# Optimization experiments

Measured on AMD Instinct MI355X. Metric: run time of the kernel, lower is better.

Reference implementation:

```python
import jax, jax.numpy as jnp
import numpy as np
from jax import lax

B, S, H = 2, 512, 2048          # batch, seq, hidden_size
I = 768                          # moe_intermediate_size
E = 64                           # num_experts
K = 8                            # num_experts_per_tok (top_k)


def setup_inputs() -> dict:
    key = jax.random.key(0)
    k1, k2, k3, k4 = jax.random.split(key, 4)
    hidden_states = jax.random.normal(k1, (B, S, H), jnp.float32)
    gate_weight = jax.random.normal(k2, (E, H), jnp.float32) * 0.02
    gate_up_weights = jax.random.normal(k3, (E, H, 2 * I), jnp.float32) * 0.02
    down_weights = jax.random.normal(k4, (E, I, H), jnp.float32) * 0.02
    return {
        "hidden_states": hidden_states,
        "gate_weight": gate_weight,
        "gate_up_weights": gate_up_weights,
        "down_weights": down_weights,
    }


def reference(hidden_states, gate_weight, gate_up_weights, down_weights):
    orig_shape = hidden_states.shape
    x = hidden_states.reshape(-1, H)          # [T, H]
    T = x.shape[0]

    # Router: softmax in fp32, top-k, renormalize (norm_topk_prob=True)
    logits = x @ gate_weight.T                # [T, E]
    probs = jax.nn.softmax(logits.astype(jnp.float32), axis=-1)
    routing_weights, selected_experts = lax.top_k(probs, K)   # [T, K]
    wsum = routing_weights.sum(axis=-1, keepdims=True)
    wsum = jnp.where(wsum == 0, 1.0, wsum)
    routing_weights = (routing_weights / wsum).astype(x.dtype)

    # Dense combine matrix [T, E]: zero weight for unselected experts.
    combine = jnp.zeros((T, E), x.dtype).at[
        jnp.arange(T)[:, None], selected_experts
    ].add(routing_weights)

    # Scan over experts; each step is one batched GEMM over all tokens,
    # masked/weighted by the combine weights (same math as per-token loop).
    def body(acc, ws):
        wgu, wd, we = ws                      # [H,2I], [I,H], [T]
        gu = x @ wgu                          # [T, 2I]
        gate, up = jnp.split(gu, 2, axis=-1)  # [T, I] each
        act = jax.nn.silu(gate) * up          # SwiGLU
        out = act @ wd                        # [T, H]
        return acc + we[:, None] * out, None

    init = jnp.zeros_like(x)
    final, _ = lax.scan(body, init, (gate_up_weights, down_weights, combine.T))
    return final.reshape(orig_shape)
```

## Files before the change

kernel.cpp:

```cpp
#include <hip/hip_runtime.h>
#include <hip/hip_bf16.h>
#include <hip/hip_fp16.h>

typedef unsigned int uint32;
typedef unsigned short u16;

#define TOK 1024
#define HID 2048
#define NEXP 64
#define TOPK 8
#define IMED 768
#define IMED2 1536

typedef __attribute__((ext_vector_type(8))) _Float16 half8;
typedef __attribute__((ext_vector_type(4))) float f32x4;
typedef __attribute__((ext_vector_type(4))) float nf4;

static __device__ __forceinline__ uint32 pack2(float a, float b) {
  union { _Float16 h[2]; uint32 u; } p;
  p.h[0] = (_Float16)a; p.h[1] = (_Float16)b;
  return p.u;
}
static __device__ __forceinline__ u16 f2h(float a) {
  union { _Float16 h; u16 u; } p;
  p.h = (_Float16)a;
  return p.u;
}

__global__ __launch_bounds__(256) void router_kernel(
    const float* __restrict__ x, const float* __restrict__ gw,
    int* __restrict__ topk_id, float* __restrict__ topk_w,
    u16* __restrict__ xh) {
  int t0 = blockIdx.x << 2;
  __shared__ float part[4][NEXP][5];
  int tid = threadIdx.x;
  int e = tid & 63, p = tid >> 6;
  const float* gwp = gw + (size_t)e * HID + (p << 9);
  const float* xp = x + (size_t)t0 * HID + (p << 9);
  float acc[4] = {0.f, 0.f, 0.f, 0.f};
  for (int i = 0; i < 128; i++) {
    float4 w = ((const float4*)gwp)[i];
    #pragma unroll
    for (int t = 0; t < 4; t++) {
      float4 xv = *(const float4*)(xp + (size_t)t * HID + (i << 2));
      acc[t] += w.x * xv.x + w.y * xv.y + w.z * xv.z + w.w * xv.w;
    }
  }
  #pragma unroll
  for (int t = 0; t < 4; t++) part[p][e][t] = acc[t];
  for (int i = tid; i < 2048; i += 256) {
    int r = i >> 9;
    int c = i & 511;
    float4 v = *(const float4*)(x + (size_t)(t0 + r) * HID + (c << 2));
    uint2 hp;
    hp.x = pack2(v.x, v.y);
    hp.y = pack2(v.z, v.w);
    *(uint2*)(xh + (size_t)(t0 + r) * HID + (c << 2)) = hp;
  }
  __syncthreads();
  int wv = tid >> 6, l = tid & 63;
  int t = t0 + wv;
  float lg = part[0][l][wv] + part[1][l][wv] + part[2][l][wv] + part[3][l][wv];
  float m = lg;
  #pragma unroll
  for (int d = 1; d < 64; d <<= 1) m = fmaxf(m, __shfl_xor(m, d));
  float v = __expf(lg - m);
  float w8[TOPK]; int i8[TOPK]; float wsum = 0.f;
  #pragma unroll
  for (int k = 0; k < TOPK; k++) {
    float bv = v; int bi = l;
    #pragma unroll
    for (int d = 1; d < 64; d <<= 1) {
      float ov = __shfl_xor(bv, d);
      int oi = __shfl_xor(bi, d);
      if (ov > bv || (ov == bv && oi < bi)) { bv = ov; bi = oi; }
    }
    w8[k] = bv; i8[k] = bi; wsum += bv;
    if (l == bi) v = -1.f;
  }
  if (l == 0) {
    float rinv = 1.f / wsum;
    #pragma unroll
    for (int k = 0; k < TOPK; k++) {
      topk_id[t * TOPK + k] = i8[k];
      topk_w[t * TOPK + k] = w8[k] * rinv;
    }
  }
}

__global__ __launch_bounds__(256) void scatter_kernel(
    const int* __restrict__ topk_id, const float* __restrict__ topk_w,
    int* __restrict__ off, int* __restrict__ gcnt,
    int* __restrict__ row_tok, float* __restrict__ row_w) {
  int e = blockIdx.x;
  __shared__ int lcnt[NEXP];
  __shared__ int sbase;
  __shared__ int scur;
  int tid = threadIdx.x;
  if (tid < NEXP) lcnt[tid] = 0;
  __syncthreads();
  for (int i = tid; i < TOK * TOPK; i += 256) atomicAdd(&lcnt[topk_id[i]], 1);
  __syncthreads();
  if (tid < 64) {
    int c = lcnt[tid];
    int xv = c;
    #pragma unroll
    for (int d = 1; d < 64; d <<= 1) {
      int y = __shfl_up(xv, d);
      if (tid >= d) xv += y;
    }
    if (tid == e) {
      sbase = xv - c;
      off[e] = xv - c;
      gcnt[e] = c;
    }
    if (tid == 0) scur = 0;
  }
  __syncthreads();
  int base = sbase;
  for (int i = tid; i < TOK * TOPK; i += 256) {
    if (topk_id[i] == e) {
      int p = atomicAdd(&scur, 1);
      row_tok[base + p] = i >> 3;
      row_w[base + p] = topk_w[i];
    }
  }
}

__global__ __launch_bounds__(512, 2) void gateup_kernel(
    const u16* __restrict__ xh, const float* __restrict__ Wgu,
    const int* __restrict__ off, const int* __restrict__ cnt,
    const int* __restrict__ row_tok, u16* __restrict__ act) {
  int bid = blockIdx.x;
  int xcd = bid & 7, s2 = bid >> 3;
  int e = xcd + ((s2 & 7) << 3);
  int slab = s2 >> 3;
  int r0 = off[e];
  int ne = cnt[e];
  int c0 = slab * 96;

  __shared__ __align__(16) char AsB[256 * 80];
  __shared__ __align__(16) char BsB[192 * 80];

  int tid = threadIdx.x;
  int lane = tid & 63;
  int wid = tid >> 6;
  int wm = wid >> 1, wn = wid & 1;
  int fr = lane & 15, hi = lane >> 4;

  int arow = tid >> 1, aseg = tid & 1;
  int tok = row_tok[r0 + ((arow < ne) ? arow : 0)];
  const u16* xa = xh + (size_t)tok * HID + (aseg << 4);
  int axr = (arow >> 2) & 3;

  bool bact = tid < 384;
  int cg = tid % 24, h = (tid / 24) & 1, kq = tid / 48;
  int bcol = cg << 2;
  int gc = h ? (IMED + c0 + bcol) : (c0 + bcol);
  const float* wb = Wgu + (size_t)e * ((size_t)HID * IMED2) + (size_t)(kq << 2) * IMED2 + gc;
  int brbase = 96 * h + bcol;

  f32x4 accg[4][3], accu[4][3];
  #pragma unroll
  for (int a = 0; a < 4; a++)
    #pragma unroll
    for (int b = 0; b < 3; b++) { accg[a][b] = (f32x4)0.f; accu[a][b] = (f32x4)0.f; }

  uint4 qa0, qa1;
  nf4 w0, w1, w2, w3;
  auto LOADT = [&]() {
    const uint4* p = (const uint4*)xa;
    qa0 = p[0]; qa1 = p[1];
    xa += 32;
    if (bact) {
      w0 = __builtin_nontemporal_load((const nf4*)(wb));
      w1 = __builtin_nontemporal_load((const nf4*)(wb + IMED2));
      w2 = __builtin_nontemporal_load((const nf4*)(wb + 2 * IMED2));
      w3 = __builtin_nontemporal_load((const nf4*)(wb + 3 * IMED2));
    }
    wb += (size_t)32 * IMED2;
  };
  auto STORET = [&]() {
    char* A_ = AsB + arow * 80;
    int g0 = aseg << 1;
    *(uint4*)(A_ + (((g0 + 0) ^ axr) << 4)) = qa0;
    *(uint4*)(A_ + (((g0 + 1) ^ axr) << 4)) = qa1;
    if (bact) {
      float c0v[4] = {w0.x, w0.y, w0.z, w0.w};
      float c1v[4] = {w1.x, w1.y, w1.z, w1.w};
      float c2v[4] = {w2.x, w2.y, w2.z, w2.w};
      float c3v[4] = {w3.x, w3.y, w3.z, w3.w};
      int kg = kq >> 1, kb = (kq & 1) << 3;
      #pragma unroll
      for (int cc = 0; cc < 4; cc++) {
        int br = brbase + cc;
        uint2 pv;
        pv.x = pack2(c0v[cc], c1v[cc]);
        pv.y = pack2(c2v[cc], c3v[cc]);
        *(uint2*)(BsB + br * 80 + (((kg ^ (br >> 2)) & 3) << 4) + kb) = pv;
      }
    }
  };

  const int NK = HID / 32;
  LOADT();
  STORET();
  LOADT();
  __syncthreads();

  for (int t = 0; t < NK; ++t) {
    half8 af[4];
    #pragma unroll
    for (int mi = 0; mi < 4; mi++) {
      int r = (wm << 6) + (mi << 4) + fr;
      af[mi] = *(half8*)(AsB + r * 80 + (((hi ^ (r >> 2)) & 3) << 4));
    }
    #pragma unroll
    for (int ni = 0; ni < 3; ni++) {
      int ng = (wn * 48) + (ni << 4) + fr;
      int nu = ng + 96;
      half8 bg = *(half8*)(BsB + ng * 80 + (((hi ^ (ng >> 2)) & 3) << 4));
      half8 bu = *(half8*)(BsB + nu * 80 + (((hi ^ (nu >> 2)) & 3) << 4));
      #pragma unroll
      for (int mi = 0; mi < 4; mi++) {
        accg[mi][ni] = __builtin_amdgcn_mfma_f32_16x16x32_f16(af[mi], bg, accg[mi][ni], 0, 0, 0);
        accu[mi][ni] = __builtin_amdgcn_mfma_f32_16x16x32_f16(af[mi], bu, accu[mi][ni], 0, 0, 0);
      }
    }
    __syncthreads();
    if (t + 1 < NK) {
      STORET();
      if (t + 2 < NK) LOADT();
      __syncthreads();
    }
  }

  #pragma unroll
  for (int mi = 0; mi < 4; mi++) {
    #pragma unroll
    for (int ni = 0; ni < 3; ni++) {
      int col = c0 + wn * 48 + (ni << 4) + fr;
      #pragma unroll
      for (int r = 0; r < 4; r++) {
        int rr = (wm << 6) + (mi << 4) + (hi << 2) + r;
        if (rr < ne) {
          float g = accg[mi][ni][r];
          float u = accu[mi][ni][r];
          float s = g / (1.f + __expf(-g)) * u;
          act[(size_t)(r0 + rr) * IMED + col] = f2h(s);
        }
      }
    }
  }
}

__global__ __launch_bounds__(512, 2) void down_kernel(
    const u16* __restrict__ act, const float* __restrict__ Wd,
    const int* __restrict__ off, const int* __restrict__ cnt,
    const int* __restrict__ row_tok, const float* __restrict__ row_w,
    float* __restrict__ out) {
  int bid = blockIdx.x;
  int xcd = bid & 7, s2 = bid >> 3;
  int e = xcd + ((s2 & 7) << 3);
  int slab = s2 >> 3;
  int r0 = off[e];
  int ne = cnt[e];
  int n0 = slab << 8;

  __shared__ __align__(16) char AsB[256 * 80];
  __shared__ __align__(16) char BsB[256 * 80];

  int tid = threadIdx.x;
  int lane = tid & 63;
  int wid = tid >> 6;
  int wm = wid >> 1, wn = wid & 1;
  int fr = lane & 15, hi = lane >> 4;

  int arow = tid >> 1, aseg = tid & 1;
  const u16* ap = act + (size_t)(r0 + ((arow < ne) ? arow : 0)) * IMED + (aseg << 4);
  int axr = (arow >> 2) & 3;

  int cq = tid & 63, kq = tid >> 6;
  int bcol = cq << 2;
  const float* wb = Wd + (size_t)e * ((size_t)IMED * HID) + (size_t)(kq << 2) * HID + n0 + bcol;

  f32x4 acc[4][8];
  #pragma unroll
  for (int a = 0; a < 4; a++)
    #pragma unroll
    for (int b = 0; b < 8; b++) acc[a][b] = (f32x4)0.f;

  uint4 qa0, qa1;
  nf4 w0, w1, w2, w3;
  auto LOADT = [&]() {
    const uint4* p = (const uint4*)ap;
    qa0 = p[0]; qa1 = p[1];
    ap += 32;
    w0 = __builtin_nontemporal_load((const nf4*)(wb));
    w1 = __builtin_nontemporal_load((const nf4*)(wb + HID));
    w2 = __builtin_nontemporal_load((const nf4*)(wb + 2 * HID));
    w3 = __builtin_nontemporal_load((const nf4*)(wb + 3 * HID));
    wb += (size_t)32 * HID;
  };
  auto STORET = [&]() {
    char* A_ = AsB + arow * 80;
    int g0 = aseg << 1;
    *(uint4*)(A_ + (((g0 + 0) ^ axr) << 4)) = qa0;
    *(uint4*)(A_ + (((g0 + 1) ^ axr) << 4)) = qa1;
    float c0v[4] = {w0.x, w0.y, w0.z, w0.w};
    float c1v[4] = {w1.x, w1.y, w1.z, w1.w};
    float c2v[4] = {w2.x, w2.y, w2.z, w2.w};
    float c3v[4] = {w3.x, w3.y, w3.z, w3.w};
    int kg = kq >> 1, kb = (kq & 1) << 3;
    #pragma unroll
    for (int cc = 0; cc < 4; cc++) {
      int br = bcol + cc;
      uint2 pv;
      pv.x = pack2(c0v[cc], c1v[cc]);
      pv.y = pack2(c2v[cc], c3v[cc]);
      *(uint2*)(BsB + br * 80 + (((kg ^ (br >> 2)) & 3) << 4) + kb) = pv;
    }
  };

  const int NK = IMED / 32;
  LOADT();
  STORET();
  LOADT();
  __syncthreads();

  for (int t = 0; t < NK; ++t) {
    half8 af[4];
    #pragma unroll
    for (int mi = 0; mi < 4; mi++) {
      int r = (wm << 6) + (mi << 4) + fr;
      af[mi] = *(half8*)(AsB + r * 80 + (((hi ^ (r >> 2)) & 3) << 4));
    }
    #pragma unroll
    for (int ni = 0; ni < 8; ni++) {
      int n = (wn << 7) + (ni << 4) + fr;
      half8 bf_ = *(half8*)(BsB + n * 80 + (((hi ^ (n >> 2)) & 3) << 4));
      #pragma unroll
      for (int mi = 0; mi < 4; mi++)
        acc[mi][ni] = __builtin_amdgcn_mfma_f32_16x16x32_f16(af[mi], bf_, acc[mi][ni], 0, 0, 0);
    }
    __syncthreads();
    if (t + 1 < NK) {
      STORET();
      if (t + 2 < NK) LOADT();
      __syncthreads();
    }
  }

  #pragma unroll
  for (int mi = 0; mi < 4; mi++) {
    #pragma unroll
    for (int r = 0; r < 4; r++) {
      int rr = (wm << 6) + (mi << 4) + (hi << 2) + r;
      if (rr < ne) {
        float w = row_w[r0 + rr];
        int t = row_tok[r0 + rr];
        #pragma unroll
        for (int ni = 0; ni < 8; ni++) {
          int col = n0 + (wn << 7) + (ni << 4) + fr;
          unsafeAtomicAdd(&out[(size_t)t * HID + col], acc[mi][ni][r] * w);
        }
      }
    }
  }
}

extern "C" void kernel_launch(void* const* d_in, const int* in_sizes, int n_in,
                              void* d_out, int out_size, void* d_ws, size_t ws_size,
                              hipStream_t stream) {
  const float* x = (const float*)d_in[0];
  const float* gw = (const float*)d_in[1];
  const float* wgu = (const float*)d_in[2];
  const float* wd = (const float*)d_in[3];
  float* out = (float*)d_out;
  char* ws = (char*)d_ws;

  int* gcnt = (int*)(ws + 0);
  int* off = (int*)(ws + 512);
  int* topk_id = (int*)(ws + 1024);
  float* topk_w = (float*)(ws + 1024 + 32768);
  int* row_tok = (int*)(ws + 1024 + 65536);
  float* row_w = (float*)(ws + 1024 + 98304);
  u16* act = (u16*)(ws + 135168);
  u16* xh = (u16*)(ws + 135168 + 12582912);

  router_kernel<<<TOK / 4, 256, 0, stream>>>(x, gw, topk_id, topk_w, xh);
  scatter_kernel<<<NEXP, 256, 0, stream>>>(topk_id, topk_w, off, gcnt, row_tok, row_w);
  (void)hipMemsetAsync(out, 0, (size_t)TOK * HID * sizeof(float), stream);
  gateup_kernel<<<512, 512, 0, stream>>>(xh, wgu, off, gcnt, row_tok, act);
  down_kernel<<<512, 512, 0, stream>>>(act, wd, off, gcnt, row_tok, row_w, out);
}
```

Measured before the change: 370.4 us.

## Fuse gate-up and down GEMMs into one persistent kernel with per-expert barrier

Merges the gate_up and down kernels into a single launch of 256 blocks. Each block computes two gate_up column slabs for its expert, then spins on a per-expert atomic counter until all four blocks of that expert finish before running two down-projection slabs. This removes a kernel launch and lets experts move to the down phase independently, at the cost of half as many blocks in flight and a spin barrier that relies on all 256 blocks being co-resident. Weight loads also switch from nontemporal to plain loads.

Measured after the change: 516.6 us. 39.5% more time.

```diff
diff --git a/kernel.cpp b/kernel.cpp
--- a/kernel.cpp
+++ b/kernel.cpp
@@ -14,7 +14,6 @@
 
 typedef __attribute__((ext_vector_type(8))) _Float16 half8;
 typedef __attribute__((ext_vector_type(4))) float f32x4;
-typedef __attribute__((ext_vector_type(4))) float nf4;
 
 static __device__ __forceinline__ uint32 pack2(float a, float b) {
   union { _Float16 h[2]; uint32 u; } p;
@@ -91,13 +90,15 @@
 __global__ __launch_bounds__(256) void scatter_kernel(
     const int* __restrict__ topk_id, const float* __restrict__ topk_w,
     int* __restrict__ off, int* __restrict__ gcnt,
-    int* __restrict__ row_tok, float* __restrict__ row_w) {
+    int* __restrict__ row_tok, float* __restrict__ row_w,
+    int* __restrict__ done) {
   int e = blockIdx.x;
   __shared__ int lcnt[NEXP];
   __shared__ int sbase;
   __shared__ int scur;
   int tid = threadIdx.x;
   if (tid < NEXP) lcnt[tid] = 0;
+  if (blockIdx.x == 0 && tid < NEXP) done[tid] = 0;
   __syncthreads();
   for (int i = tid; i < TOK * TOPK; i += 256) atomicAdd(&lcnt[topk_id[i]], 1);
   __syncthreads();
@@ -127,20 +128,21 @@
   }
 }
 
-__global__ __launch_bounds__(512, 2) void gateup_kernel(
+__global__ __launch_bounds__(512, 2) void moe_kernel(
     const u16* __restrict__ xh, const float* __restrict__ Wgu,
-    const int* __restrict__ off, const int* __restrict__ cnt,
-    const int* __restrict__ row_tok, u16* __restrict__ act) {
+    const float* __restrict__ Wd, const int* __restrict__ off,
+    const int* __restrict__ cnt, const int* __restrict__ row_tok,
+    const float* __restrict__ row_w, u16* __restrict__ act,
+    float* __restrict__ out, int* __restrict__ done) {
   int bid = blockIdx.x;
-  int xcd = bid & 7, s2 = bid >> 3;
-  int e = xcd + ((s2 & 7) << 3);
-  int slab = s2 >> 3;
+  int xcd = bid & 7, eg = (bid >> 3) & 7, q = bid >> 6;
+  int e = xcd + (eg << 3);
   int r0 = off[e];
   int ne = cnt[e];
-  int c0 = slab * 96;
-
-  __shared__ __align__(16) char AsB[256 * 80];
-  __shared__ __align__(16) char BsB[192 * 80];
+
+  __shared__ __align__(16) char LDS[40960];
+  char* AsB = LDS;
+  char* BsB = LDS + 20480;
 
   int tid = threadIdx.x;
   int lane = tid & 63;
@@ -149,222 +151,222 @@
   int fr = lane & 15, hi = lane >> 4;
 
   int arow = tid >> 1, aseg = tid & 1;
+  int axr = (arow >> 2) & 3;
   int tok = row_tok[r0 + ((arow < ne) ? arow : 0)];
-  const u16* xa = xh + (size_t)tok * HID + (aseg << 4);
-  int axr = (arow >> 2) & 3;
-
-  bool bact = tid < 384;
-  int cg = tid % 24, h = (tid / 24) & 1, kq = tid / 48;
-  int bcol = cg << 2;
-  int gc = h ? (IMED + c0 + bcol) : (c0 + bcol);
-  const float* wb = Wgu + (size_t)e * ((size_t)HID * IMED2) + (size_t)(kq << 2) * IMED2 + gc;
-  int brbase = 96 * h + bcol;
-
-  f32x4 accg[4][3], accu[4][3];
-  #pragma unroll
-  for (int a = 0; a < 4; a++)
-    #pragma unroll
-    for (int b = 0; b < 3; b++) { accg[a][b] = (f32x4)0.f; accu[a][b] = (f32x4)0.f; }
-
-  uint4 qa0, qa1;
-  nf4 w0, w1, w2, w3;
-  auto LOADT = [&]() {
-    const uint4* p = (const uint4*)xa;
-    qa0 = p[0]; qa1 = p[1];
-    xa += 32;
-    if (bact) {
-      w0 = __builtin_nontemporal_load((const nf4*)(wb));
-      w1 = __builtin_nontemporal_load((const nf4*)(wb + IMED2));
-      w2 = __builtin_nontemporal_load((const nf4*)(wb + 2 * IMED2));
-      w3 = __builtin_nontemporal_load((const nf4*)(wb + 3 * IMED2));
-    }
-    wb += (size_t)32 * IMED2;
-  };
-  auto STORET = [&]() {
-    char* A_ = AsB + arow * 80;
-    int g0 = aseg << 1;
-    *(uint4*)(A_ + (((g0 + 0) ^ axr) << 4)) = qa0;
-    *(uint4*)(A_ + (((g0 + 1) ^ axr) << 4)) = qa1;
-    if (bact) {
-      float c0v[4] = {w0.x, w0.y, w0.z, w0.w};
-      float c1v[4] = {w1.x, w1.y, w1.z, w1.w};
-      float c2v[4] = {w2.x, w2.y, w2.z, w2.w};
-      float c3v[4] = {w3.x, w3.y, w3.z, w3.w};
-      int kg = kq >> 1, kb = (kq & 1) << 3;
+
+  {
+    bool bact = tid < 384;
+    int cg = tid % 24, h = (tid / 24) & 1, kq = tid / 48;
+    int bcol = cg << 2;
+    int brbase = 96 * h + bcol;
+
+    for (int sl = 0; sl < 2; sl++) {
+      int c0 = (q + (sl << 2)) * 96;
+      const u16* xa = xh + (size_t)tok * HID + (aseg << 4);
+      int gc = h ? (IMED + c0 + bcol) : (c0 + bcol);
+      const float* wb = Wgu + (size_t)e * ((size_t)HID * IMED2) +
+                        (size_t)(kq << 2) * IMED2 + gc;
+
+      f32x4 accg[4][3], accu[4][3];
       #pragma unroll
-      for (int cc = 0; cc < 4; cc++) {
-        int br = brbase + cc;
-        uint2 pv;
-        pv.x = pack2(c0v[cc], c1v[cc]);
-        pv.y = pack2(c2v[cc], c3v[cc]);
-        *(uint2*)(BsB + br * 80 + (((kg ^ (br >> 2)) & 3) << 4) + kb) = pv;
+      for (int a = 0; a < 4; a++)
+        #pragma unroll
+        for (int b = 0; b < 3; b++) { accg[a][b] = (f32x4)0.f; accu[a][b] = (f32x4)0.f; }
+
+      uint4 qa0, qa1;
+      float4 w0, w1, w2, w3;
+      auto LOADT = [&]() {
+        const uint4* p = (const uint4*)xa;
+        qa0 = p[0]; qa1 = p[1];
+        xa += 32;
+        if (bact) {
+          w0 = *(const float4*)(wb);
+          w1 = *(const float4*)(wb + IMED2);
+          w2 = *(const float4*)(wb + 2 * IMED2);
+          w3 = *(const float4*)(wb + 3 * IMED2);
+        }
+        wb += (size_t)32 * IMED2;
+      };
+      auto STORET = [&]() {
+        char* A_ = AsB + arow * 80;
+        int g0 = aseg << 1;
+        *(uint4*)(A_ + (((g0 + 0) ^ axr) << 4)) = qa0;
+        *(uint4*)(A_ + (((g0 + 1) ^ axr) << 4)) = qa1;
+        if (bact) {
+          float c0v[4] = {w0.x, w0.y, w0.z, w0.w};
+          float c1v[4] = {w1.x, w1.y, w1.z, w1.w};
+          float c2v[4] = {w2.x, w2.y, w2.z, w2.w};
+          float c3v[4] = {w3.x, w3.y, w3.z, w3.w};
+          int kg = kq >> 1, kb = (kq & 1) << 3;
+          #pragma unroll
+          for (int cc = 0; cc < 4; cc++) {
+            int br = brbase + cc;
+            uint2 pv;
+            pv.x = pack2(c0v[cc], c1v[cc]);
+            pv.y = pack2(c2v[cc], c3v[cc]);
+            *(uint2*)(BsB + br * 80 + (((kg ^ (br >> 2)) & 3) << 4) + kb) = pv;
+          }
+        }
+      };
+
+      const int NK = HID / 32;
+      LOADT();
+      STORET();
+      LOADT();
+      __syncthreads();
+
+      for (int t = 0; t < NK; ++t) {
+        half8 af[4];
+        #pragma unroll
+        for (int mi = 0; mi < 4; mi++) {
+          int r = (wm << 6) + (mi << 4) + fr;
+          af[mi] = *(half8*)(AsB + r * 80 + (((hi ^ (r >> 2)) & 3) << 4));
+        }
+        #pragma unroll
+        for (int ni = 0; ni < 3; ni++) {
+          int ng = (wn * 48) + (ni << 4) + fr;
+          int nu = ng + 96;
+          half8 bg = *(half8*)(BsB + ng * 80 + (((hi ^ (ng >> 2)) & 3) << 4));
+          half8 bu = *(half8*)(BsB + nu * 80 + (((hi ^ (nu >> 2)) & 3) << 4));
+          #pragma unroll
+          for (int mi = 0; mi < 4; mi++) {
+            accg[mi][ni] = __builtin_amdgcn_mfma_f32_16x16x32_f16(af[mi], bg, accg[mi][ni], 0, 0, 0);
+            accu[mi][ni] = __builtin_amdgcn_mfma_f32_16x16x32_f16(af[mi], bu, accu[mi][ni], 0, 0, 0);
+          }
+        }
+        __syncthreads();
+        if (t + 1 < NK) {
+          STORET();
+          if (t + 2 < NK) LOADT();
+          __syncthreads();
+        }
       }
-    }
-  };
-
-  const int NK = HID / 32;
-  LOADT();
-  STORET();
-  LOADT();
-  __syncthreads();
-
-  for (int t = 0; t < NK; ++t) {
-    half8 af[4];
-    #pragma unroll
-    for (int mi = 0; mi < 4; mi++) {
-      int r = (wm << 6) + (mi << 4) + fr;
-      af[mi] = *(half8*)(AsB + r * 80 + (((hi ^ (r >> 2)) & 3) << 4));
-    }
-    #pragma unroll
-    for (int ni = 0; ni < 3; ni++) {
-      int ng = (wn * 48) + (ni << 4) + fr;
-      int nu = ng + 96;
-      half8 bg = *(half8*)(BsB + ng * 80 + (((hi ^ (ng >> 2)) & 3) << 4));
-      half8 bu = *(half8*)(BsB + nu * 80 + (((hi ^ (nu >> 2)) & 3) << 4));
+
       #pragma unroll
       for (int mi = 0; mi < 4; mi++) {
-        accg[mi][ni] = __builtin_amdgcn_mfma_f32_16x16x32_f16(af[mi], bg, accg[mi][ni], 0, 0, 0);
-        accu[mi][ni] = __builtin_amdgcn_mfma_f32_16x16x32_f16(af[mi], bu, accu[mi][ni], 0, 0, 0);
+        #pragma unroll
+        for (int ni = 0; ni < 3; ni++) {
+          int col = c0 + wn * 48 + (ni << 4) + fr;
+          #pragma unroll
+          for (int r = 0; r < 4; r++) {
+            int rr = (wm << 6) + (mi << 4) + (hi << 2) + r;
+            if (rr < ne) {
+              float g = accg[mi][ni][r];
+              float u = accu[mi][ni][r];
+              float s = g / (1.f + __expf(-g)) * u;
+              act[(size_t)(r0 + rr) * IMED + col] = f2h(s);
+            }
+          }
+        }
       }
-    }
-    __syncthreads();
-    if (t + 1 < NK) {
+      __syncthreads();
+    }
+  }
+
+  __threadfence();
+  __syncthreads();
+  if (tid == 0) {
+    atomicAdd(&done[e], 1);
+    while (__hip_atomic_load(done + e, __ATOMIC_ACQUIRE, __HIP_MEMORY_SCOPE_AGENT) < 4) {
+    }
+  }
+  __syncthreads();
+  __threadfence();
+
+  {
+    int cq = tid & 63, kq = tid >> 6;
+    int bcol = cq << 2;
+
+    for (int sl = 0; sl < 2; sl++) {
+      int n0 = (q + (sl << 2)) << 8;
+      const u16* ap = act + (size_t)(r0 + ((arow < ne) ? arow : 0)) * IMED + (aseg << 4);
+      const float* wb = Wd + (size_t)e * ((size_t)IMED * HID) +
+                        (size_t)(kq << 2) * HID + n0 + bcol;
+
+      f32x4 acc[4][8];
+      #pragma unroll
+      for (int a = 0; a < 4; a++)
+        #pragma unroll
+        for (int b = 0; b < 8; b++) acc[a][b] = (f32x4)0.f;
+
+      uint4 qa0, qa1;
+      float4 w0, w1, w2, w3;
+      auto LOADT = [&]() {
+        const uint4* p = (const uint4*)ap;
+        qa0 = p[0]; qa1 = p[1];
+        ap += 32;
+        w0 = *(const float4*)(wb);
+        w1 = *(const float4*)(wb + HID);
+        w2 = *(const float4*)(wb + 2 * HID);
+        w3 = *(const float4*)(wb + 3 * HID);
+        wb += (size_t)32 * HID;
+      };
+      auto STORET = [&]() {
+        char* A_ = AsB + arow * 80;
+        int g0 = aseg << 1;
+        *(uint4*)(A_ + (((g0 + 0) ^ axr) << 4)) = qa0;
+        *(uint4*)(A_ + (((g0 + 1) ^ axr) << 4)) = qa1;
+        float c0v[4] = {w0.x, w0.y, w0.z, w0.w};
+        float c1v[4] = {w1.x, w1.y, w1.z, w1.w};
+        float c2v[4] = {w2.x, w2.y, w2.z, w2.w};
+        float c3v[4] = {w3.x, w3.y, w3.z, w3.w};
+        int kg = kq >> 1, kb = (kq & 1) << 3;
+        #pragma unroll
+        for (int cc = 0; cc < 4; cc++) {
+          int br = bcol + cc;
+          uint2 pv;
+          pv.x = pack2(c0v[cc], c1v[cc]);
+          pv.y = pack2(c2v[cc], c3v[cc]);
+          *(uint2*)(BsB + br * 80 + (((kg ^ (br >> 2)) & 3) << 4) + kb) = pv;
+        }
+      };
+
+      const int NK = IMED / 32;
+      LOADT();
       STORET();
-      if (t + 2 < NK) LOADT();
+      LOADT();
       __syncthreads();
-    }
-  }
-
-  #pragma unroll
-  for (int mi = 0; mi < 4; mi++) {
-    #pragma unroll
-    for (int ni = 0; ni < 3; ni++) {
-      int col = c0 + wn * 48 + (ni << 4) + fr;
+
+      for (int t = 0; t < NK; ++t) {
+        half8 af[4];
+        #pragma unroll
+        for (int mi = 0; mi < 4; mi++) {
+          int r = (wm << 6) + (mi << 4) + fr;
+          af[mi] = *(half8*)(AsB + r * 80 + (((hi ^ (r >> 2)) & 3) << 4));
+        }
+        #pragma unroll
+        for (int ni = 0; ni < 8; ni++) {
+          int n = (wn << 7) + (ni << 4) + fr;
+          half8 bf_ = *(half8*)(BsB + n * 80 + (((hi ^ (n >> 2)) & 3) << 4));
+          #pragma unroll
+          for (int mi = 0; mi < 4; mi++)
+            acc[mi][ni] = __builtin_amdgcn_mfma_f32_16x16x32_f16(af[mi], bf_, acc[mi][ni], 0, 0, 0);
+        }
+        __syncthreads();
+        if (t + 1 < NK) {
+          STORET();
+          if (t + 2 < NK) LOADT();
+          __syncthreads();
+        }
+      }
+
       #pragma unroll
-      for (int r = 0; r < 4; r++) {
-        int rr = (wm << 6) + (mi << 4) + (hi << 2) + r;
-        if (rr < ne) {
-          float g = accg[mi][ni][r];
-          float u = accu[mi][ni][r];
-          float s = g / (1.f + __expf(-g)) * u;
-          act[(size_t)(r0 + rr) * IMED + col] = f2h(s);
+      for (int mi = 0; mi < 4; mi++) {
+        #pragma unroll
+        for (int r = 0; r < 4; r++) {
+          int rr = (wm << 6) + (mi << 4) + (hi << 2) + r;
+          if (rr < ne) {
+            float w = row_w[r0 + rr];
+            int t = row_tok[r0 + rr];
+            #pragma unroll
+            for (int ni = 0; ni < 8; ni++) {
+              int col = n0 + (wn << 7) + (ni << 4) + fr;
+              unsafeAtomicAdd(&out[(size_t)t * HID + col], acc[mi][ni][r] * w);
+            }
+          }
         }
       }
-    }
-  }
-}
-
-__global__ __launch_bounds__(512, 2) void down_kernel(
-    const u16* __restrict__ act, const float* __restrict__ Wd,
-    const int* __restrict__ off, const int* __restrict__ cnt,
-    const int* __restrict__ row_tok, const float* __restrict__ row_w,
-    float* __restrict__ out) {
-  int bid = blockIdx.x;
-  int xcd = bid & 7, s2 = bid >> 3;
-  int e = xcd + ((s2 & 7) << 3);
-  int slab = s2 >> 3;
-  int r0 = off[e];
-  int ne = cnt[e];
-  int n0 = slab << 8;
-
-  __shared__ __align__(16) char AsB[256 * 80];
-  __shared__ __align__(16) char BsB[256 * 80];
-
-  int tid = threadIdx.x;
-  int lane = tid & 63;
-  int wid = tid >> 6;
-  int wm = wid >> 1, wn = wid & 1;
-  int fr = lane & 15, hi = lane >> 4;
-
-  int arow = tid >> 1, aseg = tid & 1;
-  const u16* ap = act + (size_t)(r0 + ((arow < ne) ? arow : 0)) * IMED + (aseg << 4);
-  int axr = (arow >> 2) & 3;
-
-  int cq = tid & 63, kq = tid >> 6;
-  int bcol = cq << 2;
-  const float* wb = Wd + (size_t)e * ((size_t)IMED * HID) + (size_t)(kq << 2) * HID + n0 + bcol;
-
-  f32x4 acc[4][8];
-  #pragma unroll
-  for (int a = 0; a < 4; a++)
-    #pragma unroll
-    for (int b = 0; b < 8; b++) acc[a][b] = (f32x4)0.f;
-
-  uint4 qa0, qa1;
-  nf4 w0, w1, w2, w3;
-  auto LOADT = [&]() {
-    const uint4* p = (const uint4*)ap;
-    qa0 = p[0]; qa1 = p[1];
-    ap += 32;
-    w0 = __builtin_nontemporal_load((const nf4*)(wb));
-    w1 = __builtin_nontemporal_load((const nf4*)(wb + HID));
-    w2 = __builtin_nontemporal_load((const nf4*)(wb + 2 * HID));
-    w3 = __builtin_nontemporal_load((const nf4*)(wb + 3 * HID));
-    wb += (size_t)32 * HID;
-  };
-  auto STORET = [&]() {
-    char* A_ = AsB + arow * 80;
-    int g0 = aseg << 1;
-    *(uint4*)(A_ + (((g0 + 0) ^ axr) << 4)) = qa0;
-    *(uint4*)(A_ + (((g0 + 1) ^ axr) << 4)) = qa1;
-    float c0v[4] = {w0.x, w0.y, w0.z, w0.w};
-    float c1v[4] = {w1.x, w1.y, w1.z, w1.w};
-    float c2v[4] = {w2.x, w2.y, w2.z, w2.w};
-    float c3v[4] = {w3.x, w3.y, w3.z, w3.w};
-    int kg = kq >> 1, kb = (kq & 1) << 3;
-    #pragma unroll
-    for (int cc = 0; cc < 4; cc++) {
-      int br = bcol + cc;
-      uint2 pv;
-      pv.x = pack2(c0v[cc], c1v[cc]);
-      pv.y = pack2(c2v[cc], c3v[cc]);
-      *(uint2*)(BsB + br * 80 + (((kg ^ (br >> 2)) & 3) << 4) + kb) = pv;
-    }
-  };
-
-  const int NK = IMED / 32;
-  LOADT();
-  STORET();
-  LOADT();
-  __syncthreads();
-
-  for (int t = 0; t < NK; ++t) {
-    half8 af[4];
-    #pragma unroll
-    for (int mi = 0; mi < 4; mi++) {
-      int r = (wm << 6) + (mi << 4) + fr;
-      af[mi] = *(half8*)(AsB + r * 80 + (((hi ^ (r >> 2)) & 3) << 4));
-    }
-    #pragma unroll
-    for (int ni = 0; ni < 8; ni++) {
-      int n = (wn << 7) + (ni << 4) + fr;
-      half8 bf_ = *(half8*)(BsB + n * 80 + (((hi ^ (n >> 2)) & 3) << 4));
-      #pragma unroll
-      for (int mi = 0; mi < 4; mi++)
-        acc[mi][ni] = __builtin_amdgcn_mfma_f32_16x16x32_f16(af[mi], bf_, acc[mi][ni], 0, 0, 0);
-    }
-    __syncthreads();
-    if (t + 1 < NK) {
-      STORET();
-      if (t + 2 < NK) LOADT();
       __syncthreads();
-    }
-  }
-
-  #pragma unroll
-  for (int mi = 0; mi < 4; mi++) {
-    #pragma unroll
-    for (int r = 0; r < 4; r++) {
-      int rr = (wm << 6) + (mi << 4) + (hi << 2) + r;
-      if (rr < ne) {
-        float w = row_w[r0 + rr];
-        int t = row_tok[r0 + rr];
-        #pragma unroll
-        for (int ni = 0; ni < 8; ni++) {
-          int col = n0 + (wn << 7) + (ni << 4) + fr;
-          unsafeAtomicAdd(&out[(size_t)t * HID + col], acc[mi][ni][r] * w);
-        }
-      }
     }
   }
 }
@@ -381,6 +383,7 @@
 
   int* gcnt = (int*)(ws + 0);
   int* off = (int*)(ws + 512);
+  int* done = (int*)(ws + 768);
   int* topk_id = (int*)(ws + 1024);
   float* topk_w = (float*)(ws + 1024 + 32768);
   int* row_tok = (int*)(ws + 1024 + 65536);
@@ -389,8 +392,7 @@
   u16* xh = (u16*)(ws + 135168 + 12582912);
 
   router_kernel<<<TOK / 4, 256, 0, stream>>>(x, gw, topk_id, topk_w, xh);
-  scatter_kernel<<<NEXP, 256, 0, stream>>>(topk_id, topk_w, off, gcnt, row_tok, row_w);
+  scatter_kernel<<<NEXP, 256, 0, stream>>>(topk_id, topk_w, off, gcnt, row_tok, row_w, done);
   (void)hipMemsetAsync(out, 0, (size_t)TOK * HID * sizeof(float), stream);
-  gateup_kernel<<<512, 512, 0, stream>>>(xh, wgu, off, gcnt, row_tok, act);
-  down_kernel<<<512, 512, 0, stream>>>(act, wd, off, gcnt, row_tok, row_w, out);
-}
+  moe_kernel<<<256, 512, 0, stream>>>(xh, wgu, wd, off, gcnt, row_tok, row_w, act, out, done);
+}
```
